# Kernel optimization log

Hardware: AMD Instinct MI355X
Metric: run time of the kernel (lower is better)

The kernel has to match this reference:

```python
import jax, jax.numpy as jnp
import numpy as np

N = 1024
H = 128


def setup_inputs() -> dict:
    key = jax.random.key(0)
    ks = jax.random.split(key, 12)
    s = 0.05
    inp = {
        "h": jax.random.normal(ks[0], (N, H), dtype=jnp.float32),
        "x": jax.random.normal(ks[1], (N, 2), dtype=jnp.float32),
        "batch": jnp.zeros((N,), dtype=jnp.int32),
        # attention projections (torch Linear: y = x @ W.T + b)
        "Wq": jax.random.normal(ks[2], (H, H), dtype=jnp.float32) * s,
        "bq": jnp.zeros((H,), dtype=jnp.float32),
        "Wk": jax.random.normal(ks[3], (H, H), dtype=jnp.float32) * s,
        "bk": jnp.zeros((H,), dtype=jnp.float32),
        "Wv": jax.random.normal(ks[4], (H, H), dtype=jnp.float32) * s,
        "bv": jnp.zeros((H,), dtype=jnp.float32),
        # edge_mlp: Linear(2,H) -> ReLU -> Linear(H,H)
        "We1": jax.random.normal(ks[5], (H, 2), dtype=jnp.float32) * s,
        "be1": jnp.zeros((H,), dtype=jnp.float32),
        "We2": jax.random.normal(ks[6], (H, H), dtype=jnp.float32) * s,
        "be2": jnp.zeros((H,), dtype=jnp.float32),
        # coord_mlp: Linear(H,1)
        "Wc": jax.random.normal(ks[7], (1, H), dtype=jnp.float32) * s,
        "bc": jnp.zeros((1,), dtype=jnp.float32),
    }
    return inp


def reference(h, x, batch, Wq, bq, Wk, bk, Wv, bv, We1, be1, We2, be2, Wc, bc):
    # rel_x[i, j] = x[i] - x[j]  -> [N, N, 2]
    rel_x = x[:, None, :] - x[None, :, :]
    # edge MLP over all pairs -> [N, N, H]
    edge_feat = jax.nn.relu(rel_x @ We1.T + be1) @ We2.T + be2
    q = h @ Wq.T + bq  # [N, H]
    k = h @ Wk.T + bk
    v = h @ Wv.T + bv
    scale = 1.0 / np.sqrt(float(H)).astype(np.float32)
    attn = jax.nn.softmax((q @ k.T) * scale, axis=-1)  # [N, N]
    agg_h = attn @ v  # [N, H]
    coord_w = edge_feat @ Wc.T + bc  # [N, N, 1]
    # weighted coordinate diffusion, summed over neighbors j (axis=1)
    delta_x = jnp.sum(attn[:, :, None] * (coord_w * rel_x), axis=1)  # [N, 2]
    return (h + agg_h, x + delta_x)
```

## Files before the change

kernel.cpp:

```cpp
#include <hip/hip_runtime.h>
#include <hip/hip_fp16.h>

#define NN 1024
#define HH 128
#define QR 2
#define TPB 1024

typedef _Float16 f16x2_t __attribute__((ext_vector_type(2)));

__device__ __forceinline__ float dot2(__half2 a, __half2 b, float c) {
#if __has_builtin(__builtin_amdgcn_fdot2)
  return __builtin_amdgcn_fdot2(__builtin_bit_cast(f16x2_t, a),
                                __builtin_bit_cast(f16x2_t, b), c, false);
#else
  return fmaf(__low2float(a), __low2float(b),
              fmaf(__high2float(a), __high2float(b), c));
#endif
}

__device__ __forceinline__ __half2 relu2(__half2 a) {
#if __has_builtin(__builtin_elementwise_max)
  f16x2_t v = __builtin_bit_cast(f16x2_t, a);
  f16x2_t z = {(_Float16)0.f, (_Float16)0.f};
  return __builtin_bit_cast(__half2, __builtin_elementwise_max(v, z));
#else
  unsigned int av = __builtin_bit_cast(unsigned int, a);
  unsigned int rv;
  asm("v_pk_max_f16 %0, %1, 0" : "=v"(rv) : "v"(av));
  return __builtin_bit_cast(__half2, rv);
#endif
}

__device__ __forceinline__ float2 wmax2(float2 v) {
#pragma unroll
  for (int off = 1; off < 64; off <<= 1) {
    v.x = fmaxf(v.x, __shfl_xor(v.x, off));
    v.y = fmaxf(v.y, __shfl_xor(v.y, off));
  }
  return v;
}
__device__ __forceinline__ float2 wsum2(float2 v) {
#pragma unroll
  for (int off = 1; off < 64; off <<= 1) {
    v.x += __shfl_xor(v.x, off);
    v.y += __shfl_xor(v.y, off);
  }
  return v;
}

__global__ __launch_bounds__(128)
void prep_kernel(const float* __restrict__ Wq, const float* __restrict__ Wk,
                 const float* __restrict__ Wv, const float* __restrict__ We1,
                 const float* __restrict__ be1, const float* __restrict__ We2,
                 const float* __restrict__ be2, const float* __restrict__ Wc,
                 const float* __restrict__ bc,
                 float* __restrict__ WqT, float* __restrict__ WkT,
                 float* __restrict__ WvT, float* __restrict__ epack,
                 float* __restrict__ c0,
                 __half2* __restrict__ aB, __half2* __restrict__ bB,
                 __half2* __restrict__ uB) {
  __shared__ float su[HH];
  const int d = blockIdx.x;
  const int o = threadIdx.x;
  WqT[d * HH + o] = Wq[o * HH + d];
  WkT[d * HH + o] = Wk[o * HH + d];
  WvT[d * HH + o] = Wv[o * HH + d];
  if (d == 0) {
    float uu = 0.f;
    for (int e = 0; e < HH; ++e) uu = fmaf(Wc[e], We2[e * HH + o], uu);
    su[o] = uu;
    epack[o * 4 + 0] = We1[2 * o];
    epack[o * 4 + 1] = We1[2 * o + 1];
    epack[o * 4 + 2] = be1[o];
    epack[o * 4 + 3] = uu;
    if (o == 0) {
      float s = bc[0];
      for (int e = 0; e < HH; ++e) s = fmaf(Wc[e], be2[e], s);
      c0[0] = s;
    }
    __syncthreads();
    if (o < 64) {
      aB[o] = __halves2half2(__float2half(We1[4 * o]), __float2half(We1[4 * o + 2]));
      bB[o] = __halves2half2(__float2half(We1[4 * o + 1]), __float2half(We1[4 * o + 3]));
      uB[o] = __halves2half2(__float2half(su[2 * o]), __float2half(su[2 * o + 1]));
    }
  }
}

__global__ __launch_bounds__(128)
void qkv_kernel(const float* __restrict__ hin,
                const float* __restrict__ WqT, const float* __restrict__ WkT,
                const float* __restrict__ WvT,
                const float* __restrict__ bq, const float* __restrict__ bk,
                const float* __restrict__ bv,
                __half* __restrict__ q16, __half* __restrict__ kP,
                __half* __restrict__ v16) {
  __shared__ __align__(16) float hT[HH][QR];
  const int tid = threadIdx.x;
  const int i0 = blockIdx.x * QR;
#pragma unroll
  for (int r = 0; r < QR; ++r) hT[tid][r] = hin[(i0 + r) * HH + tid];
  __syncthreads();
  float qa0 = 0.f, qa1 = 0.f, ka0 = 0.f, ka1 = 0.f, va0 = 0.f, va1 = 0.f;
#pragma unroll 4
  for (int d = 0; d < HH; ++d) {
    float wq = WqT[d * HH + tid];
    float wk = WkT[d * HH + tid];
    float wv = WvT[d * HH + tid];
    float2 hh = *(const float2*)&hT[d][0];
    qa0 = fmaf(hh.x, wq, qa0); qa1 = fmaf(hh.y, wq, qa1);
    ka0 = fmaf(hh.x, wk, ka0); ka1 = fmaf(hh.y, wk, ka1);
    va0 = fmaf(hh.x, wv, va0); va1 = fmaf(hh.y, wv, va1);
  }
  const float scale = 0.08838834764831845f;
  float bqv = bq[tid], bkv = bk[tid], bvv = bv[tid];
  q16[(i0 + 0) * HH + tid] = __float2half((qa0 + bqv) * scale);
  q16[(i0 + 1) * HH + tid] = __float2half((qa1 + bqv) * scale);
  v16[(i0 + 0) * HH + tid] = __float2half(va0 + bvv);
  v16[(i0 + 1) * HH + tid] = __float2half(va1 + bvv);
  float kb0 = ka0 + bkv, kb1 = ka1 + bkv;
  float pr0 = __shfl_xor(kb0, 1);
  float pr1 = __shfl_xor(kb1, 1);
  if ((tid & 1) == 0) {
    const int dp = tid >> 1;
    __half2 w0 = __halves2half2(__float2half(kb0), __float2half(pr0));
    __half2 w1 = __halves2half2(__float2half(kb1), __float2half(pr1));
    *(__half2*)&kP[dp * (2 * NN) + 2 * i0]     = w0;
    *(__half2*)&kP[dp * (2 * NN) + 2 * i0 + 2] = w1;
  }
}

__global__ __launch_bounds__(TPB, 8)
void fused_kernel(const __half* __restrict__ q16, const __half* __restrict__ kP,
                  const __half* __restrict__ v16, const float* __restrict__ hin,
                  const float* __restrict__ x, const float* __restrict__ epack,
                  const __half2* __restrict__ aB, const __half2* __restrict__ bB,
                  const __half2* __restrict__ uB, const float* __restrict__ c0p,
                  float* __restrict__ out_h, float* __restrict__ out_x) {
  __shared__ __align__(16) float spA[NN];
  __shared__ __align__(16) float spB[NN];
  __shared__ __align__(16) float4 sredh[16][64];
  __shared__ __half2 stabA[64];
  __shared__ __half2 stabB[64];
  __shared__ float2 sredm[16], sreds[16], sredx[16], sredy[16];

  const int tid = threadIdx.x;
  const int lane = tid & 63;
  const int wid = tid >> 6;
  const int i0 = blockIdx.x * 2;
  const int j = tid;

  if (tid < 64) {
    const float4 ea = ((const float4*)epack)[2 * tid];
    const float4 eb = ((const float4*)epack)[2 * tid + 1];
    float x0x = x[i0 * 2 + 0], x0y = x[i0 * 2 + 1];
    float x1x = x[i0 * 2 + 2], x1y = x[i0 * 2 + 3];
    stabA[tid] = __halves2half2(
        __float2half(fmaf(ea.x, x0x, fmaf(ea.y, x0y, ea.z))),
        __float2half(fmaf(eb.x, x0x, fmaf(eb.y, x0y, eb.z))));
    stabB[tid] = __halves2half2(
        __float2half(fmaf(ea.x, x1x, fmaf(ea.y, x1y, ea.z))),
        __float2half(fmaf(eb.x, x1x, fmaf(eb.y, x1y, eb.z))));
  }

  const __half2* q0p = (const __half2*)(q16 + (i0 + 0) * HH);
  const __half2* q1p = (const __half2*)(q16 + (i0 + 1) * HH);
  float s0 = 0.f, s1 = 0.f;
#pragma unroll 8
  for (int dp = 0; dp < HH / 2; ++dp) {
    __half2 kk = *(const __half2*)&kP[dp * (2 * NN) + 2 * j];
    s0 = dot2(kk, q0p[dp], s0);
    s1 = dot2(kk, q1p[dp], s1);
  }

  float2 mv = wmax2(make_float2(s0, s1));
  if (lane == 0) sredm[wid] = mv;
  __syncthreads();
  float2 mm = sredm[0];
#pragma unroll
  for (int w2 = 1; w2 < 16; ++w2) {
    float2 t2 = sredm[w2];
    mm.x = fmaxf(mm.x, t2.x); mm.y = fmaxf(mm.y, t2.y);
  }

  float e0 = __expf(s0 - mm.x), e1 = __expf(s1 - mm.y);
  spA[j] = e0; spB[j] = e1;
  float2 sv = wsum2(make_float2(e0, e1));
  if (lane == 0) sreds[wid] = sv;
  __syncthreads();
  float2 ssv = sreds[0];
#pragma unroll
  for (int w2 = 1; w2 < 16; ++w2) { ssv.x += sreds[w2].x; ssv.y += sreds[w2].y; }
  const float inv0 = 1.f / ssv.x, inv1 = 1.f / ssv.y;

  {
    const int op = tid & 63;
    const int c = tid >> 6;
    float hA0 = 0.f, hB0 = 0.f, hA1 = 0.f, hB1 = 0.f;
#pragma unroll 4
    for (int jj = 0; jj < NN / 16; ++jj) {
      int jv = c * (NN / 16) + jj;
      __half2 vv = *(const __half2*)&v16[jv * HH + 2 * op];
      float vx = __low2float(vv), vy = __high2float(vv);
      float p0 = spA[jv];
      float p1 = spB[jv];
      hA0 = fmaf(p0, vx, hA0); hB0 = fmaf(p0, vy, hB0);
      hA1 = fmaf(p1, vx, hA1); hB1 = fmaf(p1, vy, hB1);
    }
    sredh[c][op] = make_float4(hA0, hB0, hA1, hB1);
  }

  float2 xj = *(const float2*)&x[2 * j];
  __half2 xjx2 = __float2half2_rn(xj.x);
  __half2 xjy2 = __float2half2_rn(xj.y);
  float wa0 = 0.f, wa1 = 0.f;
#pragma unroll 8
  for (int tp = 0; tp < 64; ++tp) {
    __half2 a2 = aB[tp], b2 = bB[tp], u2 = uB[tp];
    __half2 w2 = __hfma2(a2, xjx2, __hmul2(b2, xjy2));
    wa0 = dot2(u2, relu2(__hsub2(stabA[tp], w2)), wa0);
    wa1 = dot2(u2, relu2(__hsub2(stabB[tp], w2)), wa1);
  }
  const float c0v = c0p[0];
  float cw0 = e0 * (wa0 + c0v);
  float cw1 = e1 * (wa1 + c0v);
  float xi0x = x[i0 * 2 + 0], xi0y = x[i0 * 2 + 1];
  float xi1x = x[i0 * 2 + 2], xi1y = x[i0 * 2 + 3];
  float2 rx = wsum2(make_float2(cw0 * (xi0x - xj.x), cw1 * (xi1x - xj.x)));
  float2 ry = wsum2(make_float2(cw0 * (xi0y - xj.y), cw1 * (xi1y - xj.y)));
  if (lane == 0) { sredx[wid] = rx; sredy[wid] = ry; }

  __syncthreads();

  if (tid < 2 * HH) {
    const int r = tid >> 7, o = tid & 127;
    float hv = 0.f;
#pragma unroll
    for (int c2 = 0; c2 < 16; ++c2)
      hv += ((const float*)&sredh[c2][o >> 1])[(r << 1) | (o & 1)];
    float invr = r ? inv1 : inv0;
    out_h[(i0 + r) * HH + o] = hin[(i0 + r) * HH + o] + hv * invr;
  }
  if (tid < 2) {
    float sx = 0.f, sy = 0.f;
#pragma unroll
    for (int w2 = 0; w2 < 16; ++w2) {
      sx += tid ? sredx[w2].y : sredx[w2].x;
      sy += tid ? sredy[w2].y : sredy[w2].x;
    }
    float invr = tid ? inv1 : inv0;
    out_x[(i0 + tid) * 2 + 0] = x[(i0 + tid) * 2 + 0] + sx * invr;
    out_x[(i0 + tid) * 2 + 1] = x[(i0 + tid) * 2 + 1] + sy * invr;
  }
}

extern "C" void kernel_launch(void* const* d_in, const int* in_sizes, int n_in,
                              void* d_out, int out_size, void* d_ws, size_t ws_size,
                              hipStream_t stream) {
  (void)in_sizes; (void)n_in; (void)out_size; (void)ws_size;
  const float* h   = (const float*)d_in[0];
  const float* x   = (const float*)d_in[1];
  const float* Wq  = (const float*)d_in[3];
  const float* bq  = (const float*)d_in[4];
  const float* Wk  = (const float*)d_in[5];
  const float* bk  = (const float*)d_in[6];
  const float* Wv  = (const float*)d_in[7];
  const float* bv  = (const float*)d_in[8];
  const float* We1 = (const float*)d_in[9];
  const float* be1 = (const float*)d_in[10];
  const float* We2 = (const float*)d_in[11];
  const float* be2 = (const float*)d_in[12];
  const float* Wc  = (const float*)d_in[13];
  const float* bc  = (const float*)d_in[14];

  float* ws   = (float*)d_ws;
  float* WqT  = ws;
  float* WkT  = WqT + HH * HH;
  float* WvT  = WkT + HH * HH;
  float* ep   = WvT + HH * HH;
  float* c0   = ep + 4 * HH;
  __half* q16 = (__half*)(c0 + 8);
  __half* kP  = q16 + NN * HH;
  __half* v16 = kP + NN * HH;
  __half2* aB = (__half2*)(v16 + NN * HH);
  __half2* bB = aB + 64;
  __half2* uB = bB + 64;

  float* out_h = (float*)d_out;
  float* out_x = out_h + NN * HH;

  prep_kernel<<<dim3(HH), dim3(128), 0, stream>>>(
      Wq, Wk, Wv, We1, be1, We2, be2, Wc, bc, WqT, WkT, WvT, ep, c0, aB, bB, uB);
  qkv_kernel<<<dim3(NN / QR), dim3(128), 0, stream>>>(
      h, WqT, WkT, WvT, bq, bk, bv, q16, kP, v16);
  fused_kernel<<<dim3(NN / 2), dim3(TPB), 0, stream>>>(
      q16, kP, v16, h, x, ep, aB, bB, uB, c0, out_h, out_x);
}
```

Measured before the change: 135.9 us.

## Process four query rows per block and read K row-major with vector loads

Each fused block now handles four query rows instead of two, so every K, V and edge-MLP value loaded per j is reused across twice as many rows, and the grid halves to 256 blocks. K is stored row-major, and each thread reads its own key row with 16-byte vector loads in place of the previous strided packed-pair layout. The cost is more registers and shared memory per block (launch bounds lowered to 4 waves), and only 256 blocks on a device with many CUs, which may reduce parallelism. The per-thread K-row loads are also uncoalesced across threads.

```diff
diff --git a/kernel.cpp b/kernel.cpp
--- a/kernel.cpp
+++ b/kernel.cpp
@@ -5,6 +5,7 @@
 #define HH 128
 #define QR 2
 #define TPB 1024
+#define RPB 4
 
 typedef _Float16 f16x2_t __attribute__((ext_vector_type(2)));
 
@@ -31,19 +32,23 @@
 #endif
 }
 
-__device__ __forceinline__ float2 wmax2(float2 v) {
+__device__ __forceinline__ float4 wmax4(float4 v) {
 #pragma unroll
   for (int off = 1; off < 64; off <<= 1) {
     v.x = fmaxf(v.x, __shfl_xor(v.x, off));
     v.y = fmaxf(v.y, __shfl_xor(v.y, off));
+    v.z = fmaxf(v.z, __shfl_xor(v.z, off));
+    v.w = fmaxf(v.w, __shfl_xor(v.w, off));
   }
   return v;
 }
-__device__ __forceinline__ float2 wsum2(float2 v) {
+__device__ __forceinline__ float4 wsum4(float4 v) {
 #pragma unroll
   for (int off = 1; off < 64; off <<= 1) {
     v.x += __shfl_xor(v.x, off);
     v.y += __shfl_xor(v.y, off);
+    v.z += __shfl_xor(v.z, off);
+    v.w += __shfl_xor(v.w, off);
   }
   return v;
 }
@@ -93,7 +98,7 @@
                 const float* __restrict__ WvT,
                 const float* __restrict__ bq, const float* __restrict__ bk,
                 const float* __restrict__ bv,
-                __half* __restrict__ q16, __half* __restrict__ kP,
+                __half* __restrict__ q16, __half* __restrict__ k16,
                 __half* __restrict__ v16) {
   __shared__ __align__(16) float hT[HH][QR];
   const int tid = threadIdx.x;
@@ -116,141 +121,160 @@
   float bqv = bq[tid], bkv = bk[tid], bvv = bv[tid];
   q16[(i0 + 0) * HH + tid] = __float2half((qa0 + bqv) * scale);
   q16[(i0 + 1) * HH + tid] = __float2half((qa1 + bqv) * scale);
+  k16[(i0 + 0) * HH + tid] = __float2half(ka0 + bkv);
+  k16[(i0 + 1) * HH + tid] = __float2half(ka1 + bkv);
   v16[(i0 + 0) * HH + tid] = __float2half(va0 + bvv);
   v16[(i0 + 1) * HH + tid] = __float2half(va1 + bvv);
-  float kb0 = ka0 + bkv, kb1 = ka1 + bkv;
-  float pr0 = __shfl_xor(kb0, 1);
-  float pr1 = __shfl_xor(kb1, 1);
-  if ((tid & 1) == 0) {
-    const int dp = tid >> 1;
-    __half2 w0 = __halves2half2(__float2half(kb0), __float2half(pr0));
-    __half2 w1 = __halves2half2(__float2half(kb1), __float2half(pr1));
-    *(__half2*)&kP[dp * (2 * NN) + 2 * i0]     = w0;
-    *(__half2*)&kP[dp * (2 * NN) + 2 * i0 + 2] = w1;
-  }
-}
-
-__global__ __launch_bounds__(TPB, 8)
-void fused_kernel(const __half* __restrict__ q16, const __half* __restrict__ kP,
+}
+
+__global__ __launch_bounds__(TPB, 4)
+void fused_kernel(const __half* __restrict__ q16, const __half* __restrict__ k16,
                   const __half* __restrict__ v16, const float* __restrict__ hin,
                   const float* __restrict__ x, const float* __restrict__ epack,
                   const __half2* __restrict__ aB, const __half2* __restrict__ bB,
                   const __half2* __restrict__ uB, const float* __restrict__ c0p,
                   float* __restrict__ out_h, float* __restrict__ out_x) {
-  __shared__ __align__(16) float spA[NN];
-  __shared__ __align__(16) float spB[NN];
-  __shared__ __align__(16) float4 sredh[16][64];
-  __shared__ __half2 stabA[64];
-  __shared__ __half2 stabB[64];
-  __shared__ float2 sredm[16], sreds[16], sredx[16], sredy[16];
+  __shared__ __align__(16) float4 sp[NN];
+  __shared__ __align__(16) float4 sredh[16][HH];
+  __shared__ __half2 stab[RPB][64];
+  __shared__ float4 sredm[16], sreds[16], sredx[16], sredy[16];
 
   const int tid = threadIdx.x;
   const int lane = tid & 63;
   const int wid = tid >> 6;
-  const int i0 = blockIdx.x * 2;
+  const int i0 = blockIdx.x * RPB;
   const int j = tid;
 
-  if (tid < 64) {
-    const float4 ea = ((const float4*)epack)[2 * tid];
-    const float4 eb = ((const float4*)epack)[2 * tid + 1];
-    float x0x = x[i0 * 2 + 0], x0y = x[i0 * 2 + 1];
-    float x1x = x[i0 * 2 + 2], x1y = x[i0 * 2 + 3];
-    stabA[tid] = __halves2half2(
-        __float2half(fmaf(ea.x, x0x, fmaf(ea.y, x0y, ea.z))),
-        __float2half(fmaf(eb.x, x0x, fmaf(eb.y, x0y, eb.z))));
-    stabB[tid] = __halves2half2(
-        __float2half(fmaf(ea.x, x1x, fmaf(ea.y, x1y, ea.z))),
-        __float2half(fmaf(eb.x, x1x, fmaf(eb.y, x1y, eb.z))));
-  }
-
-  const __half2* q0p = (const __half2*)(q16 + (i0 + 0) * HH);
-  const __half2* q1p = (const __half2*)(q16 + (i0 + 1) * HH);
-  float s0 = 0.f, s1 = 0.f;
-#pragma unroll 8
-  for (int dp = 0; dp < HH / 2; ++dp) {
-    __half2 kk = *(const __half2*)&kP[dp * (2 * NN) + 2 * j];
-    s0 = dot2(kk, q0p[dp], s0);
-    s1 = dot2(kk, q1p[dp], s1);
-  }
-
-  float2 mv = wmax2(make_float2(s0, s1));
+  if (tid < 4 * 64) {
+    const int r = tid & 3, tp = tid >> 2;
+    const float4 ea = ((const float4*)epack)[2 * tp];
+    const float4 eb = ((const float4*)epack)[2 * tp + 1];
+    float xrx = x[(i0 + r) * 2 + 0], xry = x[(i0 + r) * 2 + 1];
+    stab[r][tp] = __halves2half2(
+        __float2half(fmaf(ea.x, xrx, fmaf(ea.y, xry, ea.z))),
+        __float2half(fmaf(eb.x, xrx, fmaf(eb.y, xry, eb.z))));
+  }
+
+  const float4* kr4 = (const float4*)(k16 + (size_t)j * HH);
+  const __half2* q0p = (const __half2*)(q16 + (size_t)(i0 + 0) * HH);
+  const __half2* q1p = (const __half2*)(q16 + (size_t)(i0 + 1) * HH);
+  const __half2* q2p = (const __half2*)(q16 + (size_t)(i0 + 2) * HH);
+  const __half2* q3p = (const __half2*)(q16 + (size_t)(i0 + 3) * HH);
+  float s0 = 0.f, s1 = 0.f, s2 = 0.f, s3 = 0.f;
+#pragma unroll
+  for (int c = 0; c < 16; ++c) {
+    float4 raw = kr4[c];
+    __half2 k0 = __builtin_bit_cast(__half2, raw.x);
+    __half2 k1 = __builtin_bit_cast(__half2, raw.y);
+    __half2 k2 = __builtin_bit_cast(__half2, raw.z);
+    __half2 k3 = __builtin_bit_cast(__half2, raw.w);
+    const int dp = 4 * c;
+    s0 = dot2(k0, q0p[dp], s0); s0 = dot2(k1, q0p[dp + 1], s0);
+    s0 = dot2(k2, q0p[dp + 2], s0); s0 = dot2(k3, q0p[dp + 3], s0);
+    s1 = dot2(k0, q1p[dp], s1); s1 = dot2(k1, q1p[dp + 1], s1);
+    s1 = dot2(k2, q1p[dp + 2], s1); s1 = dot2(k3, q1p[dp + 3], s1);
+    s2 = dot2(k0, q2p[dp], s2); s2 = dot2(k1, q2p[dp + 1], s2);
+    s2 = dot2(k2, q2p[dp + 2], s2); s2 = dot2(k3, q2p[dp + 3], s2);
+    s3 = dot2(k0, q3p[dp], s3); s3 = dot2(k1, q3p[dp + 1], s3);
+    s3 = dot2(k2, q3p[dp + 2], s3); s3 = dot2(k3, q3p[dp + 3], s3);
+  }
+
+  float4 mv = wmax4(make_float4(s0, s1, s2, s3));
   if (lane == 0) sredm[wid] = mv;
   __syncthreads();
-  float2 mm = sredm[0];
+  float4 mm = sredm[0];
 #pragma unroll
   for (int w2 = 1; w2 < 16; ++w2) {
-    float2 t2 = sredm[w2];
-    mm.x = fmaxf(mm.x, t2.x); mm.y = fmaxf(mm.y, t2.y);
+    float4 t4 = sredm[w2];
+    mm.x = fmaxf(mm.x, t4.x); mm.y = fmaxf(mm.y, t4.y);
+    mm.z = fmaxf(mm.z, t4.z); mm.w = fmaxf(mm.w, t4.w);
   }
 
   float e0 = __expf(s0 - mm.x), e1 = __expf(s1 - mm.y);
-  spA[j] = e0; spB[j] = e1;
-  float2 sv = wsum2(make_float2(e0, e1));
+  float e2 = __expf(s2 - mm.z), e3 = __expf(s3 - mm.w);
+  sp[j] = make_float4(e0, e1, e2, e3);
+  float4 sv = wsum4(make_float4(e0, e1, e2, e3));
   if (lane == 0) sreds[wid] = sv;
   __syncthreads();
-  float2 ssv = sreds[0];
-#pragma unroll
-  for (int w2 = 1; w2 < 16; ++w2) { ssv.x += sreds[w2].x; ssv.y += sreds[w2].y; }
-  const float inv0 = 1.f / ssv.x, inv1 = 1.f / ssv.y;
+  float4 ssv = sreds[0];
+#pragma unroll
+  for (int w2 = 1; w2 < 16; ++w2) {
+    float4 t4 = sreds[w2];
+    ssv.x += t4.x; ssv.y += t4.y; ssv.z += t4.z; ssv.w += t4.w;
+  }
+  const float4 inv4 = make_float4(1.f / ssv.x, 1.f / ssv.y, 1.f / ssv.z, 1.f / ssv.w);
 
   {
     const int op = tid & 63;
-    const int c = tid >> 6;
-    float hA0 = 0.f, hB0 = 0.f, hA1 = 0.f, hB1 = 0.f;
+    const int cc = tid >> 6;
+    float hA0 = 0.f, hA1 = 0.f, hA2 = 0.f, hA3 = 0.f;
+    float hB0 = 0.f, hB1 = 0.f, hB2 = 0.f, hB3 = 0.f;
 #pragma unroll 4
     for (int jj = 0; jj < NN / 16; ++jj) {
-      int jv = c * (NN / 16) + jj;
+      int jv = cc * (NN / 16) + jj;
       __half2 vv = *(const __half2*)&v16[jv * HH + 2 * op];
       float vx = __low2float(vv), vy = __high2float(vv);
-      float p0 = spA[jv];
-      float p1 = spB[jv];
-      hA0 = fmaf(p0, vx, hA0); hB0 = fmaf(p0, vy, hB0);
-      hA1 = fmaf(p1, vx, hA1); hB1 = fmaf(p1, vy, hB1);
-    }
-    sredh[c][op] = make_float4(hA0, hB0, hA1, hB1);
+      float4 pp = sp[jv];
+      hA0 = fmaf(pp.x, vx, hA0); hB0 = fmaf(pp.x, vy, hB0);
+      hA1 = fmaf(pp.y, vx, hA1); hB1 = fmaf(pp.y, vy, hB1);
+      hA2 = fmaf(pp.z, vx, hA2); hB2 = fmaf(pp.z, vy, hB2);
+      hA3 = fmaf(pp.w, vx, hA3); hB3 = fmaf(pp.w, vy, hB3);
+    }
+    sredh[cc][2 * op + 0] = make_float4(hA0, hA1, hA2, hA3);
+    sredh[cc][2 * op + 1] = make_float4(hB0, hB1, hB2, hB3);
   }
 
   float2 xj = *(const float2*)&x[2 * j];
   __half2 xjx2 = __float2half2_rn(xj.x);
   __half2 xjy2 = __float2half2_rn(xj.y);
-  float wa0 = 0.f, wa1 = 0.f;
+  float wa0 = 0.f, wa1 = 0.f, wa2 = 0.f, wa3 = 0.f;
 #pragma unroll 8
   for (int tp = 0; tp < 64; ++tp) {
     __half2 a2 = aB[tp], b2 = bB[tp], u2 = uB[tp];
-    __half2 w2 = __hfma2(a2, xjx2, __hmul2(b2, xjy2));
-    wa0 = dot2(u2, relu2(__hsub2(stabA[tp], w2)), wa0);
-    wa1 = dot2(u2, relu2(__hsub2(stabB[tp], w2)), wa1);
+    __half2 w2h = __hfma2(a2, xjx2, __hmul2(b2, xjy2));
+    wa0 = dot2(u2, relu2(__hsub2(stab[0][tp], w2h)), wa0);
+    wa1 = dot2(u2, relu2(__hsub2(stab[1][tp], w2h)), wa1);
+    wa2 = dot2(u2, relu2(__hsub2(stab[2][tp], w2h)), wa2);
+    wa3 = dot2(u2, relu2(__hsub2(stab[3][tp], w2h)), wa3);
   }
   const float c0v = c0p[0];
-  float cw0 = e0 * (wa0 + c0v);
-  float cw1 = e1 * (wa1 + c0v);
-  float xi0x = x[i0 * 2 + 0], xi0y = x[i0 * 2 + 1];
-  float xi1x = x[i0 * 2 + 2], xi1y = x[i0 * 2 + 3];
-  float2 rx = wsum2(make_float2(cw0 * (xi0x - xj.x), cw1 * (xi1x - xj.x)));
-  float2 ry = wsum2(make_float2(cw0 * (xi0y - xj.y), cw1 * (xi1y - xj.y)));
+  float cw0 = e0 * (wa0 + c0v), cw1 = e1 * (wa1 + c0v);
+  float cw2 = e2 * (wa2 + c0v), cw3 = e3 * (wa3 + c0v);
+  float xi0x = x[(i0 + 0) * 2 + 0], xi0y = x[(i0 + 0) * 2 + 1];
+  float xi1x = x[(i0 + 1) * 2 + 0], xi1y = x[(i0 + 1) * 2 + 1];
+  float xi2x = x[(i0 + 2) * 2 + 0], xi2y = x[(i0 + 2) * 2 + 1];
+  float xi3x = x[(i0 + 3) * 2 + 0], xi3y = x[(i0 + 3) * 2 + 1];
+  float4 rx = wsum4(make_float4(cw0 * (xi0x - xj.x), cw1 * (xi1x - xj.x),
+                                cw2 * (xi2x - xj.x), cw3 * (xi3x - xj.x)));
+  float4 ry = wsum4(make_float4(cw0 * (xi0y - xj.y), cw1 * (xi1y - xj.y),
+                                cw2 * (xi2y - xj.y), cw3 * (xi3y - xj.y)));
   if (lane == 0) { sredx[wid] = rx; sredy[wid] = ry; }
 
   __syncthreads();
 
-  if (tid < 2 * HH) {
-    const int r = tid >> 7, o = tid & 127;
-    float hv = 0.f;
-#pragma unroll
-    for (int c2 = 0; c2 < 16; ++c2)
-      hv += ((const float*)&sredh[c2][o >> 1])[(r << 1) | (o & 1)];
-    float invr = r ? inv1 : inv0;
-    out_h[(i0 + r) * HH + o] = hin[(i0 + r) * HH + o] + hv * invr;
-  }
-  if (tid < 2) {
+  if (tid < HH) {
+    float4 acc = sredh[0][tid];
+#pragma unroll
+    for (int c2 = 1; c2 < 16; ++c2) {
+      float4 t4 = sredh[c2][tid];
+      acc.x += t4.x; acc.y += t4.y; acc.z += t4.z; acc.w += t4.w;
+    }
+    out_h[(i0 + 0) * HH + tid] = hin[(i0 + 0) * HH + tid] + acc.x * inv4.x;
+    out_h[(i0 + 1) * HH + tid] = hin[(i0 + 1) * HH + tid] + acc.y * inv4.y;
+    out_h[(i0 + 2) * HH + tid] = hin[(i0 + 2) * HH + tid] + acc.z * inv4.z;
+    out_h[(i0 + 3) * HH + tid] = hin[(i0 + 3) * HH + tid] + acc.w * inv4.w;
+  }
+  if (tid < 4) {
+    const int r = tid;
     float sx = 0.f, sy = 0.f;
 #pragma unroll
     for (int w2 = 0; w2 < 16; ++w2) {
-      sx += tid ? sredx[w2].y : sredx[w2].x;
-      sy += tid ? sredy[w2].y : sredy[w2].x;
-    }
-    float invr = tid ? inv1 : inv0;
-    out_x[(i0 + tid) * 2 + 0] = x[(i0 + tid) * 2 + 0] + sx * invr;
-    out_x[(i0 + tid) * 2 + 1] = x[(i0 + tid) * 2 + 1] + sy * invr;
+      sx += ((const float*)&sredx[w2])[r];
+      sy += ((const float*)&sredy[w2])[r];
+    }
+    float invr = ((const float*)&inv4)[r];
+    out_x[(i0 + r) * 2 + 0] = x[(i0 + r) * 2 + 0] + sx * invr;
+    out_x[(i0 + r) * 2 + 1] = x[(i0 + r) * 2 + 1] + sy * invr;
   }
 }
 
@@ -280,8 +304,8 @@
   float* ep   = WvT + HH * HH;
   float* c0   = ep + 4 * HH;
   __half* q16 = (__half*)(c0 + 8);
-  __half* kP  = q16 + NN * HH;
-  __half* v16 = kP + NN * HH;
+  __half* k16 = q16 + NN * HH;
+  __half* v16 = k16 + NN * HH;
   __half2* aB = (__half2*)(v16 + NN * HH);
   __half2* bB = aB + 64;
   __half2* uB = bB + 64;
@@ -292,7 +316,7 @@
   prep_kernel<<<dim3(HH), dim3(128), 0, stream>>>(
       Wq, Wk, Wv, We1, be1, We2, be2, Wc, bc, WqT, WkT, WvT, ep, c0, aB, bB, uB);
   qkv_kernel<<<dim3(NN / QR), dim3(128), 0, stream>>>(
-      h, WqT, WkT, WvT, bq, bk, bv, q16, kP, v16);
-  fused_kernel<<<dim3(NN / 2), dim3(TPB), 0, stream>>>(
-      q16, kP, v16, h, x, ep, aB, bB, uB, c0, out_h, out_x);
-}
+      h, WqT, WkT, WvT, bq, bk, bv, q16, k16, v16);
+  fused_kernel<<<dim3(NN / RPB), dim3(TPB), 0, stream>>>(
+      q16, k16, v16, h, x, ep, aB, bB, uB, c0, out_h, out_x);
+}
```

Result: slower. 152.1 us (+11.9%).

## Halve fused block size, give each thread two keys, widen K/V loads

Applied to the files above, without the earlier changes.

The fused attention kernel now runs 512 threads per block, and each thread handles two key columns j instead of one. This lets loaded q values and the edge-MLP tables be reused across two keys. K is stored in a chunked layout with 8 halves per key, so each thread reads it with float4 loads, and V is kept in fp32 so the P·V loop can read float4 rows. The cost is higher register pressure per thread, more bytes read for V, and fewer waves available to hide latency.

```diff
diff --git a/kernel.cpp b/kernel.cpp
--- a/kernel.cpp
+++ b/kernel.cpp
@@ -4,7 +4,8 @@
 #define NN 1024
 #define HH 128
 #define QR 2
-#define TPB 1024
+#define TPB 512
+#define RPB 2
 
 typedef _Float16 f16x2_t __attribute__((ext_vector_type(2)));
 
@@ -93,8 +94,8 @@
                 const float* __restrict__ WvT,
                 const float* __restrict__ bq, const float* __restrict__ bk,
                 const float* __restrict__ bv,
-                __half* __restrict__ q16, __half* __restrict__ kP,
-                __half* __restrict__ v16) {
+                __half* __restrict__ q16, __half* __restrict__ k8,
+                float* __restrict__ vF) {
   __shared__ __align__(16) float hT[HH][QR];
   const int tid = threadIdx.x;
   const int i0 = blockIdx.x * QR;
@@ -116,141 +117,164 @@
   float bqv = bq[tid], bkv = bk[tid], bvv = bv[tid];
   q16[(i0 + 0) * HH + tid] = __float2half((qa0 + bqv) * scale);
   q16[(i0 + 1) * HH + tid] = __float2half((qa1 + bqv) * scale);
-  v16[(i0 + 0) * HH + tid] = __float2half(va0 + bvv);
-  v16[(i0 + 1) * HH + tid] = __float2half(va1 + bvv);
-  float kb0 = ka0 + bkv, kb1 = ka1 + bkv;
-  float pr0 = __shfl_xor(kb0, 1);
-  float pr1 = __shfl_xor(kb1, 1);
-  if ((tid & 1) == 0) {
-    const int dp = tid >> 1;
-    __half2 w0 = __halves2half2(__float2half(kb0), __float2half(pr0));
-    __half2 w1 = __halves2half2(__float2half(kb1), __float2half(pr1));
-    *(__half2*)&kP[dp * (2 * NN) + 2 * i0]     = w0;
-    *(__half2*)&kP[dp * (2 * NN) + 2 * i0 + 2] = w1;
-  }
-}
-
-__global__ __launch_bounds__(TPB, 8)
-void fused_kernel(const __half* __restrict__ q16, const __half* __restrict__ kP,
-                  const __half* __restrict__ v16, const float* __restrict__ hin,
+  const int c = tid >> 3, slot = tid & 7;
+  k8[(size_t)((c * NN + i0 + 0) << 3) + slot] = __float2half(ka0 + bkv);
+  k8[(size_t)((c * NN + i0 + 1) << 3) + slot] = __float2half(ka1 + bkv);
+  vF[(i0 + 0) * HH + tid] = va0 + bvv;
+  vF[(i0 + 1) * HH + tid] = va1 + bvv;
+}
+
+__global__ __launch_bounds__(TPB, 4)
+void fused_kernel(const __half* __restrict__ q16, const __half* __restrict__ k8,
+                  const float* __restrict__ vF, const float* __restrict__ hin,
                   const float* __restrict__ x, const float* __restrict__ epack,
                   const __half2* __restrict__ aB, const __half2* __restrict__ bB,
                   const __half2* __restrict__ uB, const float* __restrict__ c0p,
                   float* __restrict__ out_h, float* __restrict__ out_x) {
-  __shared__ __align__(16) float spA[NN];
-  __shared__ __align__(16) float spB[NN];
-  __shared__ __align__(16) float4 sredh[16][64];
-  __shared__ __half2 stabA[64];
-  __shared__ __half2 stabB[64];
-  __shared__ float2 sredm[16], sreds[16], sredx[16], sredy[16];
+  __shared__ __align__(16) float2 sp2[NN];
+  __shared__ __align__(16) float4 sredh[16][32][2];
+  __shared__ __half2 stab[RPB][64];
+  __shared__ float2 sredm[8], sreds[8], sredx[8], sredy[8];
 
   const int tid = threadIdx.x;
   const int lane = tid & 63;
   const int wid = tid >> 6;
-  const int i0 = blockIdx.x * 2;
-  const int j = tid;
-
-  if (tid < 64) {
-    const float4 ea = ((const float4*)epack)[2 * tid];
-    const float4 eb = ((const float4*)epack)[2 * tid + 1];
-    float x0x = x[i0 * 2 + 0], x0y = x[i0 * 2 + 1];
-    float x1x = x[i0 * 2 + 2], x1y = x[i0 * 2 + 3];
-    stabA[tid] = __halves2half2(
-        __float2half(fmaf(ea.x, x0x, fmaf(ea.y, x0y, ea.z))),
-        __float2half(fmaf(eb.x, x0x, fmaf(eb.y, x0y, eb.z))));
-    stabB[tid] = __halves2half2(
-        __float2half(fmaf(ea.x, x1x, fmaf(ea.y, x1y, ea.z))),
-        __float2half(fmaf(eb.x, x1x, fmaf(eb.y, x1y, eb.z))));
-  }
-
-  const __half2* q0p = (const __half2*)(q16 + (i0 + 0) * HH);
-  const __half2* q1p = (const __half2*)(q16 + (i0 + 1) * HH);
-  float s0 = 0.f, s1 = 0.f;
-#pragma unroll 8
-  for (int dp = 0; dp < HH / 2; ++dp) {
-    __half2 kk = *(const __half2*)&kP[dp * (2 * NN) + 2 * j];
-    s0 = dot2(kk, q0p[dp], s0);
-    s1 = dot2(kk, q1p[dp], s1);
-  }
-
-  float2 mv = wmax2(make_float2(s0, s1));
+  const int i0 = blockIdx.x * RPB;
+  const int j0 = tid, j1 = tid + TPB;
+
+  if (tid < 2 * 64) {
+    const int r = tid & 1, tp = tid >> 1;
+    const float4 ea = ((const float4*)epack)[2 * tp];
+    const float4 eb = ((const float4*)epack)[2 * tp + 1];
+    float xrx = x[(i0 + r) * 2 + 0], xry = x[(i0 + r) * 2 + 1];
+    stab[r][tp] = __halves2half2(
+        __float2half(fmaf(ea.x, xrx, fmaf(ea.y, xry, ea.z))),
+        __float2half(fmaf(eb.x, xrx, fmaf(eb.y, xry, eb.z))));
+  }
+
+  const __half2* q0p = (const __half2*)(q16 + (size_t)(i0 + 0) * HH);
+  const __half2* q1p = (const __half2*)(q16 + (size_t)(i0 + 1) * HH);
+  const float4* k84 = (const float4*)k8;
+  float s00 = 0.f, s01 = 0.f, s10 = 0.f, s11 = 0.f;
+#pragma unroll
+  for (int c = 0; c < 16; ++c) {
+    float4 ka = k84[c * NN + j0];
+    float4 kb = k84[c * NN + j1];
+    __half2 a0 = __builtin_bit_cast(__half2, ka.x);
+    __half2 a1 = __builtin_bit_cast(__half2, ka.y);
+    __half2 a2 = __builtin_bit_cast(__half2, ka.z);
+    __half2 a3 = __builtin_bit_cast(__half2, ka.w);
+    __half2 b0 = __builtin_bit_cast(__half2, kb.x);
+    __half2 b1 = __builtin_bit_cast(__half2, kb.y);
+    __half2 b2 = __builtin_bit_cast(__half2, kb.z);
+    __half2 b3 = __builtin_bit_cast(__half2, kb.w);
+    __half2 qa0 = q0p[4 * c + 0], qa1 = q0p[4 * c + 1];
+    __half2 qa2 = q0p[4 * c + 2], qa3 = q0p[4 * c + 3];
+    __half2 qb0 = q1p[4 * c + 0], qb1 = q1p[4 * c + 1];
+    __half2 qb2 = q1p[4 * c + 2], qb3 = q1p[4 * c + 3];
+    s00 = dot2(a0, qa0, s00); s00 = dot2(a1, qa1, s00);
+    s00 = dot2(a2, qa2, s00); s00 = dot2(a3, qa3, s00);
+    s01 = dot2(b0, qa0, s01); s01 = dot2(b1, qa1, s01);
+    s01 = dot2(b2, qa2, s01); s01 = dot2(b3, qa3, s01);
+    s10 = dot2(a0, qb0, s10); s10 = dot2(a1, qb1, s10);
+    s10 = dot2(a2, qb2, s10); s10 = dot2(a3, qb3, s10);
+    s11 = dot2(b0, qb0, s11); s11 = dot2(b1, qb1, s11);
+    s11 = dot2(b2, qb2, s11); s11 = dot2(b3, qb3, s11);
+  }
+
+  float2 mv = wmax2(make_float2(fmaxf(s00, s01), fmaxf(s10, s11)));
   if (lane == 0) sredm[wid] = mv;
   __syncthreads();
   float2 mm = sredm[0];
 #pragma unroll
-  for (int w2 = 1; w2 < 16; ++w2) {
+  for (int w2 = 1; w2 < 8; ++w2) {
     float2 t2 = sredm[w2];
     mm.x = fmaxf(mm.x, t2.x); mm.y = fmaxf(mm.y, t2.y);
   }
 
-  float e0 = __expf(s0 - mm.x), e1 = __expf(s1 - mm.y);
-  spA[j] = e0; spB[j] = e1;
-  float2 sv = wsum2(make_float2(e0, e1));
+  float e00 = __expf(s00 - mm.x), e01 = __expf(s01 - mm.x);
+  float e10 = __expf(s10 - mm.y), e11 = __expf(s11 - mm.y);
+  sp2[j0] = make_float2(e00, e10);
+  sp2[j1] = make_float2(e01, e11);
+  float2 sv = wsum2(make_float2(e00 + e01, e10 + e11));
   if (lane == 0) sreds[wid] = sv;
   __syncthreads();
   float2 ssv = sreds[0];
 #pragma unroll
-  for (int w2 = 1; w2 < 16; ++w2) { ssv.x += sreds[w2].x; ssv.y += sreds[w2].y; }
+  for (int w2 = 1; w2 < 8; ++w2) { ssv.x += sreds[w2].x; ssv.y += sreds[w2].y; }
   const float inv0 = 1.f / ssv.x, inv1 = 1.f / ssv.y;
 
   {
-    const int op = tid & 63;
-    const int c = tid >> 6;
-    float hA0 = 0.f, hB0 = 0.f, hA1 = 0.f, hB1 = 0.f;
+    const int op2 = tid & 31;
+    const int cc = tid >> 5;
+    float4 ar0 = make_float4(0.f, 0.f, 0.f, 0.f);
+    float4 ar1 = make_float4(0.f, 0.f, 0.f, 0.f);
 #pragma unroll 4
     for (int jj = 0; jj < NN / 16; ++jj) {
-      int jv = c * (NN / 16) + jj;
-      __half2 vv = *(const __half2*)&v16[jv * HH + 2 * op];
-      float vx = __low2float(vv), vy = __high2float(vv);
-      float p0 = spA[jv];
-      float p1 = spB[jv];
-      hA0 = fmaf(p0, vx, hA0); hB0 = fmaf(p0, vy, hB0);
-      hA1 = fmaf(p1, vx, hA1); hB1 = fmaf(p1, vy, hB1);
+      int jv = cc * (NN / 16) + jj;
+      float4 vv = ((const float4*)vF)[jv * 32 + op2];
+      float2 pp = sp2[jv];
+      ar0.x = fmaf(pp.x, vv.x, ar0.x); ar0.y = fmaf(pp.x, vv.y, ar0.y);
+      ar0.z = fmaf(pp.x, vv.z, ar0.z); ar0.w = fmaf(pp.x, vv.w, ar0.w);
+      ar1.x = fmaf(pp.y, vv.x, ar1.x); ar1.y = fmaf(pp.y, vv.y, ar1.y);
+      ar1.z = fmaf(pp.y, vv.z, ar1.z); ar1.w = fmaf(pp.y, vv.w, ar1.w);
     }
-    sredh[c][op] = make_float4(hA0, hB0, hA1, hB1);
-  }
-
-  float2 xj = *(const float2*)&x[2 * j];
-  __half2 xjx2 = __float2half2_rn(xj.x);
-  __half2 xjy2 = __float2half2_rn(xj.y);
-  float wa0 = 0.f, wa1 = 0.f;
+    sredh[cc][op2][0] = ar0;
+    sredh[cc][op2][1] = ar1;
+  }
+
+  float2 xja = *(const float2*)&x[2 * j0];
+  float2 xjb = *(const float2*)&x[2 * j1];
+  __half2 xax = __float2half2_rn(xja.x), xay = __float2half2_rn(xja.y);
+  __half2 xbx = __float2half2_rn(xjb.x), xby = __float2half2_rn(xjb.y);
+  float wa00 = 0.f, wa01 = 0.f, wa10 = 0.f, wa11 = 0.f;
 #pragma unroll 8
   for (int tp = 0; tp < 64; ++tp) {
     __half2 a2 = aB[tp], b2 = bB[tp], u2 = uB[tp];
-    __half2 w2 = __hfma2(a2, xjx2, __hmul2(b2, xjy2));
-    wa0 = dot2(u2, relu2(__hsub2(stabA[tp], w2)), wa0);
-    wa1 = dot2(u2, relu2(__hsub2(stabB[tp], w2)), wa1);
+    __half2 wA = __hfma2(a2, xax, __hmul2(b2, xay));
+    __half2 wB = __hfma2(a2, xbx, __hmul2(b2, xby));
+    __half2 s0t = stab[0][tp], s1t = stab[1][tp];
+    wa00 = dot2(u2, relu2(__hsub2(s0t, wA)), wa00);
+    wa01 = dot2(u2, relu2(__hsub2(s0t, wB)), wa01);
+    wa10 = dot2(u2, relu2(__hsub2(s1t, wA)), wa10);
+    wa11 = dot2(u2, relu2(__hsub2(s1t, wB)), wa11);
   }
   const float c0v = c0p[0];
-  float cw0 = e0 * (wa0 + c0v);
-  float cw1 = e1 * (wa1 + c0v);
+  float cw00 = e00 * (wa00 + c0v), cw01 = e01 * (wa01 + c0v);
+  float cw10 = e10 * (wa10 + c0v), cw11 = e11 * (wa11 + c0v);
   float xi0x = x[i0 * 2 + 0], xi0y = x[i0 * 2 + 1];
   float xi1x = x[i0 * 2 + 2], xi1y = x[i0 * 2 + 3];
-  float2 rx = wsum2(make_float2(cw0 * (xi0x - xj.x), cw1 * (xi1x - xj.x)));
-  float2 ry = wsum2(make_float2(cw0 * (xi0y - xj.y), cw1 * (xi1y - xj.y)));
+  float2 rx = wsum2(make_float2(
+      fmaf(cw00, xi0x - xja.x, cw01 * (xi0x - xjb.x)),
+      fmaf(cw10, xi1x - xja.x, cw11 * (xi1x - xjb.x))));
+  float2 ry = wsum2(make_float2(
+      fmaf(cw00, xi0y - xja.y, cw01 * (xi0y - xjb.y)),
+      fmaf(cw10, xi1y - xja.y, cw11 * (xi1y - xjb.y))));
   if (lane == 0) { sredx[wid] = rx; sredy[wid] = ry; }
 
   __syncthreads();
 
   if (tid < 2 * HH) {
-    const int r = tid >> 7, o = tid & 127;
-    float hv = 0.f;
+    const int f = tid & 127, r = tid >> 7;
+    const int o2 = f >> 2, fi = f & 3;
+    float acc = 0.f;
 #pragma unroll
     for (int c2 = 0; c2 < 16; ++c2)
-      hv += ((const float*)&sredh[c2][o >> 1])[(r << 1) | (o & 1)];
+      acc += ((const float*)&sredh[c2][o2][r])[fi];
     float invr = r ? inv1 : inv0;
-    out_h[(i0 + r) * HH + o] = hin[(i0 + r) * HH + o] + hv * invr;
+    out_h[(i0 + r) * HH + f] = hin[(i0 + r) * HH + f] + acc * invr;
   }
   if (tid < 2) {
+    const int r = tid;
     float sx = 0.f, sy = 0.f;
 #pragma unroll
-    for (int w2 = 0; w2 < 16; ++w2) {
-      sx += tid ? sredx[w2].y : sredx[w2].x;
-      sy += tid ? sredy[w2].y : sredy[w2].x;
+    for (int w2 = 0; w2 < 8; ++w2) {
+      sx += r ? sredx[w2].y : sredx[w2].x;
+      sy += r ? sredy[w2].y : sredy[w2].x;
     }
-    float invr = tid ? inv1 : inv0;
-    out_x[(i0 + tid) * 2 + 0] = x[(i0 + tid) * 2 + 0] + sx * invr;
-    out_x[(i0 + tid) * 2 + 1] = x[(i0 + tid) * 2 + 1] + sy * invr;
+    float invr = r ? inv1 : inv0;
+    out_x[(i0 + r) * 2 + 0] = x[(i0 + r) * 2 + 0] + sx * invr;
+    out_x[(i0 + r) * 2 + 1] = x[(i0 + r) * 2 + 1] + sy * invr;
   }
 }
 
@@ -280,9 +304,9 @@
   float* ep   = WvT + HH * HH;
   float* c0   = ep + 4 * HH;
   __half* q16 = (__half*)(c0 + 8);
-  __half* kP  = q16 + NN * HH;
-  __half* v16 = kP + NN * HH;
-  __half2* aB = (__half2*)(v16 + NN * HH);
+  __half* k8  = q16 + NN * HH;
+  float* vF   = (float*)(k8 + NN * HH);
+  __half2* aB = (__half2*)(vF + NN * HH);
   __half2* bB = aB + 64;
   __half2* uB = bB + 64;
 
@@ -292,7 +316,7 @@
   prep_kernel<<<dim3(HH), dim3(128), 0, stream>>>(
       Wq, Wk, Wv, We1, be1, We2, be2, Wc, bc, WqT, WkT, WvT, ep, c0, aB, bB, uB);
   qkv_kernel<<<dim3(NN / QR), dim3(128), 0, stream>>>(
-      h, WqT, WkT, WvT, bq, bk, bv, q16, kP, v16);
-  fused_kernel<<<dim3(NN / 2), dim3(TPB), 0, stream>>>(
-      q16, kP, v16, h, x, ep, aB, bB, uB, c0, out_h, out_x);
-}
+      h, WqT, WkT, WvT, bq, bk, bv, q16, k8, vF);
+  fused_kernel<<<dim3(NN / RPB), dim3(TPB), 0, stream>>>(
+      q16, k8, vF, h, x, ep, aB, bB, uB, c0, out_h, out_x);
+}
```

After: 124.4 us. 1.09x faster.
